# Optimization experiments

Measured on AMD Instinct MI355X. Metric: run time of the kernel, lower is better.

## Reference

```python
import jax, jax.numpy as jnp
import numpy as np

B = 16384          # batch size (positions)
NNZ_PER = 32       # active features per position (pieces on board)
F = 768            # 2 colors x 6 pieces x 64 squares
H = 512            # hidden_size


def setup_inputs() -> dict:
    key = jax.random.key(0)
    k1, k2, k3, k4, k5, k6 = jax.random.split(key, 6)
    nnz = B * NNZ_PER
    batch_row = jnp.repeat(jnp.arange(B, dtype=jnp.int64), NNZ_PER)
    stm_feat = jax.random.randint(k1, (nnz,), 0, F, dtype=jnp.int64)
    nstm_feat = jax.random.randint(k2, (nnz,), 0, F, dtype=jnp.int64)
    stm_indices = jnp.stack([batch_row, stm_feat])    # [2, nnz] COO (batch, feature)
    nstm_indices = jnp.stack([batch_row, nstm_feat])  # [2, nnz]
    stm_values = jnp.ones((nnz,), dtype=jnp.float32)   # binary features
    nstm_values = jnp.ones((nnz,), dtype=jnp.float32)
    W_ft = jax.random.normal(k3, (H, F), dtype=jnp.float32) * 0.02
    b_ft = jax.random.normal(k4, (H,), dtype=jnp.float32) * 0.02
    W_out = jax.random.normal(k5, (1, 2 * H), dtype=jnp.float32) * 0.02
    b_out = jax.random.normal(k6, (1,), dtype=jnp.float32) * 0.02
    return {
        "stm_indices": stm_indices,
        "nstm_indices": nstm_indices,
        "stm_values": stm_values,
        "nstm_values": nstm_values,
        "batch_size": B,
        "W_ft": W_ft,
        "b_ft": b_ft,
        "W_out": W_out,
        "b_out": b_out,
    }


def _to_dense(indices, values, batch_size):
    # torch.sparse_coo_tensor(...).to_dense(): duplicates are summed.
    dense = jnp.zeros((batch_size, F), dtype=jnp.float32)
    return dense.at[indices[0], indices[1]].add(values)


def reference(stm_indices, nstm_indices, stm_values, nstm_values, batch_size,
              W_ft, b_ft, W_out, b_out):
    stm_dense = _to_dense(stm_indices, stm_values, batch_size)     # [B, 768]
    nstm_dense = _to_dense(nstm_indices, nstm_values, batch_size)  # [B, 768]
    stm_hidden = stm_dense @ W_ft.T + b_ft     # [B, H]
    nstm_hidden = nstm_dense @ W_ft.T + b_ft   # [B, H]
    hidden = jnp.concatenate([stm_hidden, nstm_hidden], axis=1)  # [B, 2H]
    hidden = jnp.clip(hidden, 0.0, 1.0)
    return jax.nn.sigmoid(hidden @ W_out.T + b_out)  # [B, 1]
```

## Files before the change

kernel.cpp:

```cpp
#include <hip/hip_runtime.h>
#include <hip/hip_fp16.h>

#define B_SZ    16384
#define NNZ_PER 32
#define F_DIM   768
#define H_DIM   512
#define SLICE_H 64
#define NSLICE  8
#define CHUNK   256
#define ROWB    80

typedef unsigned int  uint32;
typedef unsigned char uchar;

#define WT8_OFF  0u
#define PK_OFF   393216u
#define PART_OFF (393216u + 4194304u)

__device__ inline uchar f32_to_e5m2(float x) {
    __half h = __float2half_rn(x);
    unsigned short hb = *(unsigned short*)&h;
    unsigned short lsb = (hb >> 8) & 1;
    hb = (unsigned short)(hb + 0x7F + lsb);
    return (uchar)(hb >> 8);
}

__global__ __launch_bounds__(256) void prep(
    const float* __restrict__ W,
    const int*   __restrict__ stm_idx,
    const int*   __restrict__ nstm_idx,
    const float* __restrict__ stm_val,
    const float* __restrict__ nstm_val,
    uchar*  __restrict__ Wt8,
    uint32* __restrict__ packed)
{
    if (blockIdx.x < 384) {
        __shared__ float tile[32][33];
        const int bx = blockIdx.x % 24;
        const int by = blockIdx.x / 24;
        const int f0 = bx * 32, h0 = by * 32;
        const int tx = threadIdx.x & 31;
        const int ty = threadIdx.x >> 5;

#pragma unroll
        for (int i = 0; i < 32; i += 8)
            tile[ty + i][tx] = W[(h0 + ty + i) * F_DIM + f0 + tx];
        __syncthreads();
        const int s = h0 >> 6;
#pragma unroll
        for (int i = 0; i < 32; i += 8) {
            const int f = f0 + ty + i;
            const int h = h0 + tx;
            Wt8[(size_t)s * (F_DIM * SLICE_H) + f * SLICE_H + (h & 63)] =
                f32_to_e5m2(tile[tx][ty + i]);
        }
    } else {
        const int e = (blockIdx.x - 384) * 256 + threadIdx.x;
        const int b = e >> 6, j = e & 63;
        const int NNZ = B_SZ * NNZ_PER;
        int f; float v;
        if (j < 32) { f = stm_idx [NNZ + b * 32 + j];        v = stm_val [b * 32 + j]; }
        else        { f = nstm_idx[NNZ + b * 32 + (j - 32)]; v = nstm_val[b * 32 + (j - 32)]; }
        __half hv = __float2half_rn(v);
        packed[e] = (uint32)(unsigned short)(f * ROWB) |
                    ((uint32)(*(unsigned short*)&hv) << 16);
    }
}

__global__ __launch_bounds__(1024, 8) void nnue_main(
    const uchar*  __restrict__ Wt8,
    const uint32* __restrict__ packed,
    const float*  __restrict__ b_ft,
    const float*  __restrict__ W_out,
    float* __restrict__ partials)
{
    __shared__ uchar Wl[F_DIM * ROWB];
    const int tid   = threadIdx.x;
    const int chunk = blockIdx.x;
    const int s     = blockIdx.y;

    {
        const uchar* src = Wt8 + (size_t)s * (F_DIM * SLICE_H);
#pragma unroll
        for (int pass = 0; pass < 3; ++pass) {
            const int o = pass * 16384 + tid * 16;
            const int f = o >> 6, col = o & 63;
            uint4 v = *(const uint4*)(src + o);
            *(uint4*)(&Wl[f * ROWB + col]) = v;
        }
    }
    __syncthreads();

    const int w    = tid >> 6;
    const int lane = tid & 63;
    const int hs   = lane & 3;
    const int pl   = lane >> 2;
    const int pos  = chunk * CHUNK + w * 16 + pl;
    const int hb   = hs * 16;

    const uint4* pk4 = (const uint4*)(packed + pos * 64);

    const uint32 selA = 0x01040004u;
    const uint32 selB = 0x03040204u;

    __half2 z = __float2half2_rn(0.f);
    __half2 sa[8] = {z,z,z,z,z,z,z,z};
    __half2 na[8] = {z,z,z,z,z,z,z,z};

#define PROC1(acc, e)                                                         \
    {                                                                         \
        const uint32 off = (e & 0xFFFFu) + (uint32)hb;                        \
        uint32 vvb = __builtin_amdgcn_perm(e, e, 0x03020302u);                \
        __half2 vv = *(__half2*)&vvb;                                         \
        uint4 wv = *(const uint4*)(&Wl[off]);                                 \
        uint32 p;                                                             \
        p = __builtin_amdgcn_perm(0u, wv.x, selA); acc[0] = __hfma2(*(__half2*)&p, vv, acc[0]); \
        p = __builtin_amdgcn_perm(0u, wv.x, selB); acc[1] = __hfma2(*(__half2*)&p, vv, acc[1]); \
        p = __builtin_amdgcn_perm(0u, wv.y, selA); acc[2] = __hfma2(*(__half2*)&p, vv, acc[2]); \
        p = __builtin_amdgcn_perm(0u, wv.y, selB); acc[3] = __hfma2(*(__half2*)&p, vv, acc[3]); \
        p = __builtin_amdgcn_perm(0u, wv.z, selA); acc[4] = __hfma2(*(__half2*)&p, vv, acc[4]); \
        p = __builtin_amdgcn_perm(0u, wv.z, selB); acc[5] = __hfma2(*(__half2*)&p, vv, acc[5]); \
        p = __builtin_amdgcn_perm(0u, wv.w, selA); acc[6] = __hfma2(*(__half2*)&p, vv, acc[6]); \
        p = __builtin_amdgcn_perm(0u, wv.w, selB); acc[7] = __hfma2(*(__half2*)&p, vv, acc[7]); \
    }

#pragma unroll
    for (int jg = 0; jg < 8; ++jg) {
        uint4 cur = pk4[jg];
        PROC1(sa, cur.x); PROC1(sa, cur.y); PROC1(sa, cur.z); PROC1(sa, cur.w);
    }
#pragma unroll
    for (int jg = 8; jg < 16; ++jg) {
        uint4 cur = pk4[jg];
        PROC1(na, cur.x); PROC1(na, cur.y); PROC1(na, cur.z); PROC1(na, cur.w);
    }
#undef PROC1

    const int h0 = s * SLICE_H + hb;
    float dot = 0.f;
#pragma unroll
    for (int i = 0; i < 8; ++i) {
        float2 bi  = *(const float2*)(b_ft  + h0 + 2 * i);
        float2 wsv = *(const float2*)(W_out + h0 + 2 * i);
        float2 wnv = *(const float2*)(W_out + H_DIM + h0 + 2 * i);
        float a0 = fminf(fmaxf(__low2float (sa[i]) + bi.x, 0.f), 1.f);
        float a1 = fminf(fmaxf(__high2float(sa[i]) + bi.y, 0.f), 1.f);
        float c0 = fminf(fmaxf(__low2float (na[i]) + bi.x, 0.f), 1.f);
        float c1 = fminf(fmaxf(__high2float(na[i]) + bi.y, 0.f), 1.f);
        dot += a0 * wsv.x + a1 * wsv.y + c0 * wnv.x + c1 * wnv.y;
    }
    dot += __shfl_xor(dot, 1, 64);
    dot += __shfl_xor(dot, 2, 64);
    if (hs == 0) partials[s * B_SZ + pos] = dot;
}

__global__ __launch_bounds__(256) void finalize(
    const float* __restrict__ partials,
    const float* __restrict__ b_out,
    float* __restrict__ out)
{
    const int b = blockIdx.x * 256 + threadIdx.x;
    float a = b_out[0];
#pragma unroll
    for (int s = 0; s < NSLICE; ++s)
        a += partials[s * B_SZ + b];
    out[b] = 1.f / (1.f + expf(-a));
}

extern "C" void kernel_launch(void* const* d_in, const int* in_sizes, int n_in,
                              void* d_out, int out_size, void* d_ws, size_t ws_size,
                              hipStream_t stream) {
    const int*   stm_idx  = (const int*)  d_in[0];
    const int*   nstm_idx = (const int*)  d_in[1];
    const float* stm_val  = (const float*)d_in[2];
    const float* nstm_val = (const float*)d_in[3];
    const float* W_ft     = (const float*)d_in[5];
    const float* b_ft     = (const float*)d_in[6];
    const float* W_out    = (const float*)d_in[7];
    const float* b_out    = (const float*)d_in[8];
    float*       out      = (float*)d_out;

    uchar*  Wt8      = (uchar*) ((char*)d_ws + WT8_OFF);
    uint32* packed   = (uint32*)((char*)d_ws + PK_OFF);
    float*  partials = (float*) ((char*)d_ws + PART_OFF);

    prep<<<384 + (B_SZ * 64) / 256, 256, 0, stream>>>(
        W_ft, stm_idx, nstm_idx, stm_val, nstm_val, Wt8, packed);

    dim3 grid(B_SZ / CHUNK, NSLICE);
    nnue_main<<<grid, 1024, 0, stream>>>(Wt8, packed, b_ft, W_out, partials);

    finalize<<<B_SZ / 256, 256, 0, stream>>>(partials, b_out, out);
}
```

Before: 105.2 us.

## Bucket features by range and process all hidden units per wave with fused finalize

The prep kernel now sorts each position's active features into six 128-feature ranges, using ballot and popcount to build per-range lists and counts. The main kernel walks the ranges, staging a 128x512 e5m2 weight tile in LDS each time. Each wave covers four positions across all 512 hidden units, broadcasting list entries with readlane and reading 8 contiguous bytes per lane from LDS. The clamp, output dot, bias and sigmoid are fused into this kernel, removing the partials buffer and the finalize launch. In exchange, each block stages the full weight matrix for only 32 positions, which raises LDS fill traffic, and any range holding more than 24 features for one side is silently truncated.

After: 125.8 us. 19.7% more time.

```diff
diff --git a/kernel.cpp b/kernel.cpp
--- a/kernel.cpp
+++ b/kernel.cpp
@@ -5,17 +5,21 @@
 #define NNZ_PER 32
 #define F_DIM   768
 #define H_DIM   512
-#define SLICE_H 64
-#define NSLICE  8
-#define CHUNK   256
-#define ROWB    80
+#define NRANGE  6
+#define RF      128
+#define CAP     24
+#define LSTRIDE 48
+#define WAVES   8
+#define PPW     4
+#define POS_PER_BLOCK (WAVES * PPW)
 
 typedef unsigned int  uint32;
+typedef unsigned long long uint64;
 typedef unsigned char uchar;
 
 #define WT8_OFF  0u
-#define PK_OFF   393216u
-#define PART_OFF (393216u + 4194304u)
+#define LIST_OFF 393216u
+#define CNT_OFF  (393216u + 18874368u)
 
 __device__ inline uchar f32_to_e5m2(float x) {
     __half h = __float2half_rn(x);
@@ -32,7 +36,8 @@
     const float* __restrict__ stm_val,
     const float* __restrict__ nstm_val,
     uchar*  __restrict__ Wt8,
-    uint32* __restrict__ packed)
+    uint32* __restrict__ lists,
+    uint32* __restrict__ counts)
 {
     if (blockIdx.x < 384) {
         __shared__ float tile[32][33];
@@ -41,130 +46,155 @@
         const int f0 = bx * 32, h0 = by * 32;
         const int tx = threadIdx.x & 31;
         const int ty = threadIdx.x >> 5;
-
 #pragma unroll
         for (int i = 0; i < 32; i += 8)
             tile[ty + i][tx] = W[(h0 + ty + i) * F_DIM + f0 + tx];
         __syncthreads();
-        const int s = h0 >> 6;
-#pragma unroll
-        for (int i = 0; i < 32; i += 8) {
-            const int f = f0 + ty + i;
-            const int h = h0 + tx;
-            Wt8[(size_t)s * (F_DIM * SLICE_H) + f * SLICE_H + (h & 63)] =
+#pragma unroll
+        for (int i = 0; i < 32; i += 8)
+            Wt8[(size_t)(f0 + ty + i) * H_DIM + (h0 + tx)] =
                 f32_to_e5m2(tile[tx][ty + i]);
-        }
     } else {
-        const int e = (blockIdx.x - 384) * 256 + threadIdx.x;
-        const int b = e >> 6, j = e & 63;
-        const int NNZ = B_SZ * NNZ_PER;
+        const int wv   = threadIdx.x >> 6;
+        const int lane = threadIdx.x & 63;
+        const int pos  = (blockIdx.x - 384) * 4 + wv;
+        const int NNZ  = B_SZ * NNZ_PER;
+
         int f; float v;
-        if (j < 32) { f = stm_idx [NNZ + b * 32 + j];        v = stm_val [b * 32 + j]; }
-        else        { f = nstm_idx[NNZ + b * 32 + (j - 32)]; v = nstm_val[b * 32 + (j - 32)]; }
+        if (lane < 32) { f = stm_idx [NNZ + pos * 32 + lane];        v = stm_val [pos * 32 + lane]; }
+        else           { f = nstm_idx[NNZ + pos * 32 + (lane - 32)]; v = nstm_val[pos * 32 + (lane - 32)]; }
+        const int range = f >> 7;
         __half hv = __float2half_rn(v);
-        packed[e] = (uint32)(unsigned short)(f * ROWB) |
-                    ((uint32)(*(unsigned short*)&hv) << 16);
-    }
-}
-
-__global__ __launch_bounds__(1024, 8) void nnue_main(
+        const uint32 packed = ((uint32)(f & 127) << 9) |
+                              ((uint32)(*(unsigned short*)&hv) << 16);
+        const uint64 below = (1ull << lane) - 1;
+
+#pragma unroll
+        for (int r = 0; r < NRANGE; ++r) {
+            const uint64 m  = __ballot(range == r);
+            const uint32 ms = (uint32)m, mn = (uint32)(m >> 32);
+            if (range == r) {
+                const uint64 lower = m & below;
+                int slot = (lane < 32) ? __popc((uint32)lower)
+                                       : (CAP + __popc((uint32)(lower >> 32)));
+                if (slot < 2 * CAP)
+                    lists[(size_t)(pos * NRANGE + r) * LSTRIDE + slot] = packed;
+            }
+            if (lane == 0) {
+                int cs = __popc(ms); if (cs > CAP) cs = CAP;
+                int cn = __popc(mn); if (cn > CAP) cn = CAP;
+                counts[pos * NRANGE + r] = (uint32)cs | ((uint32)cn << 16);
+            }
+        }
+    }
+}
+
+__global__ __launch_bounds__(512, 4) void nnue_main(
     const uchar*  __restrict__ Wt8,
-    const uint32* __restrict__ packed,
+    const uint32* __restrict__ lists,
+    const uint32* __restrict__ counts,
     const float*  __restrict__ b_ft,
     const float*  __restrict__ W_out,
-    float* __restrict__ partials)
+    const float*  __restrict__ b_out,
+    float* __restrict__ out)
 {
-    __shared__ uchar Wl[F_DIM * ROWB];
+    __shared__ uchar Wl[RF * H_DIM];
     const int tid   = threadIdx.x;
-    const int chunk = blockIdx.x;
-    const int s     = blockIdx.y;
-
-    {
-        const uchar* src = Wt8 + (size_t)s * (F_DIM * SLICE_H);
-#pragma unroll
-        for (int pass = 0; pass < 3; ++pass) {
-            const int o = pass * 16384 + tid * 16;
-            const int f = o >> 6, col = o & 63;
-            uint4 v = *(const uint4*)(src + o);
-            *(uint4*)(&Wl[f * ROWB + col]) = v;
-        }
-    }
-    __syncthreads();
-
-    const int w    = tid >> 6;
-    const int lane = tid & 63;
-    const int hs   = lane & 3;
-    const int pl   = lane >> 2;
-    const int pos  = chunk * CHUNK + w * 16 + pl;
-    const int hb   = hs * 16;
-
-    const uint4* pk4 = (const uint4*)(packed + pos * 64);
+    const int wv    = tid >> 6;
+    const int lane  = tid & 63;
+    const int pbase = blockIdx.x * POS_PER_BLOCK + wv * PPW;
+    const uint32 lane8 = (uint32)lane << 3;
 
     const uint32 selA = 0x01040004u;
     const uint32 selB = 0x03040204u;
 
     __half2 z = __float2half2_rn(0.f);
-    __half2 sa[8] = {z,z,z,z,z,z,z,z};
-    __half2 na[8] = {z,z,z,z,z,z,z,z};
-
-#define PROC1(acc, e)                                                         \
-    {                                                                         \
-        const uint32 off = (e & 0xFFFFu) + (uint32)hb;                        \
-        uint32 vvb = __builtin_amdgcn_perm(e, e, 0x03020302u);                \
-        __half2 vv = *(__half2*)&vvb;                                         \
-        uint4 wv = *(const uint4*)(&Wl[off]);                                 \
-        uint32 p;                                                             \
-        p = __builtin_amdgcn_perm(0u, wv.x, selA); acc[0] = __hfma2(*(__half2*)&p, vv, acc[0]); \
-        p = __builtin_amdgcn_perm(0u, wv.x, selB); acc[1] = __hfma2(*(__half2*)&p, vv, acc[1]); \
-        p = __builtin_amdgcn_perm(0u, wv.y, selA); acc[2] = __hfma2(*(__half2*)&p, vv, acc[2]); \
-        p = __builtin_amdgcn_perm(0u, wv.y, selB); acc[3] = __hfma2(*(__half2*)&p, vv, acc[3]); \
-        p = __builtin_amdgcn_perm(0u, wv.z, selA); acc[4] = __hfma2(*(__half2*)&p, vv, acc[4]); \
-        p = __builtin_amdgcn_perm(0u, wv.z, selB); acc[5] = __hfma2(*(__half2*)&p, vv, acc[5]); \
-        p = __builtin_amdgcn_perm(0u, wv.w, selA); acc[6] = __hfma2(*(__half2*)&p, vv, acc[6]); \
-        p = __builtin_amdgcn_perm(0u, wv.w, selB); acc[7] = __hfma2(*(__half2*)&p, vv, acc[7]); \
-    }
-
-#pragma unroll
-    for (int jg = 0; jg < 8; ++jg) {
-        uint4 cur = pk4[jg];
-        PROC1(sa, cur.x); PROC1(sa, cur.y); PROC1(sa, cur.z); PROC1(sa, cur.w);
-    }
-#pragma unroll
-    for (int jg = 8; jg < 16; ++jg) {
-        uint4 cur = pk4[jg];
-        PROC1(na, cur.x); PROC1(na, cur.y); PROC1(na, cur.z); PROC1(na, cur.w);
-    }
-#undef PROC1
-
-    const int h0 = s * SLICE_H + hb;
-    float dot = 0.f;
-#pragma unroll
-    for (int i = 0; i < 8; ++i) {
-        float2 bi  = *(const float2*)(b_ft  + h0 + 2 * i);
-        float2 wsv = *(const float2*)(W_out + h0 + 2 * i);
-        float2 wnv = *(const float2*)(W_out + H_DIM + h0 + 2 * i);
-        float a0 = fminf(fmaxf(__low2float (sa[i]) + bi.x, 0.f), 1.f);
-        float a1 = fminf(fmaxf(__high2float(sa[i]) + bi.y, 0.f), 1.f);
-        float c0 = fminf(fmaxf(__low2float (na[i]) + bi.x, 0.f), 1.f);
-        float c1 = fminf(fmaxf(__high2float(na[i]) + bi.y, 0.f), 1.f);
-        dot += a0 * wsv.x + a1 * wsv.y + c0 * wnv.x + c1 * wnv.y;
-    }
-    dot += __shfl_xor(dot, 1, 64);
-    dot += __shfl_xor(dot, 2, 64);
-    if (hs == 0) partials[s * B_SZ + pos] = dot;
-}
-
-__global__ __launch_bounds__(256) void finalize(
-    const float* __restrict__ partials,
-    const float* __restrict__ b_out,
-    float* __restrict__ out)
-{
-    const int b = blockIdx.x * 256 + threadIdx.x;
-    float a = b_out[0];
-#pragma unroll
-    for (int s = 0; s < NSLICE; ++s)
-        a += partials[s * B_SZ + b];
-    out[b] = 1.f / (1.f + expf(-a));
+    __half2 sa[PPW][4], na[PPW][4];
+#pragma unroll
+    for (int p = 0; p < PPW; ++p)
+#pragma unroll
+        for (int k = 0; k < 4; ++k) { sa[p][k] = z; na[p][k] = z; }
+
+    for (int r = 0; r < NRANGE; ++r) {
+        __syncthreads();
+        {
+            const uchar* src = Wt8 + (size_t)r * (RF * H_DIM);
+#pragma unroll
+            for (int i = 0; i < 8; ++i) {
+                const int o = i * 8192 + tid * 16;
+                *(uint4*)(Wl + o) = *(const uint4*)(src + o);
+            }
+        }
+        __syncthreads();
+
+        uint32 cw[PPW], el[PPW];
+#pragma unroll
+        for (int p = 0; p < PPW; ++p) {
+            const int pr = (pbase + p) * NRANGE + r;
+            cw[p] = counts[pr];
+            el[p] = 0;
+            if (lane < 2 * CAP) el[p] = lists[(size_t)pr * LSTRIDE + lane];
+        }
+
+#pragma unroll
+        for (int p = 0; p < PPW; ++p) {
+            int cs = (int)(cw[p] & 0xFFFFu);  if (cs > CAP) cs = CAP;
+            int cn = (int)(cw[p] >> 16);      if (cn > CAP) cn = CAP;
+
+            for (int j = 0; j < cs; ++j) {
+                const uint32 e   = __builtin_amdgcn_readlane(el[p], j);
+                const uint32 off = e & 0xFFFFu;
+                uint32 vvb = (e & 0xFFFF0000u) | (e >> 16);
+                __half2 vv = *(__half2*)&vvb;
+                uint2 w2 = *(const uint2*)(Wl + off + lane8);
+                uint32 q;
+                q = __builtin_amdgcn_perm(0u, w2.x, selA); sa[p][0] = __hfma2(*(__half2*)&q, vv, sa[p][0]);
+                q = __builtin_amdgcn_perm(0u, w2.x, selB); sa[p][1] = __hfma2(*(__half2*)&q, vv, sa[p][1]);
+                q = __builtin_amdgcn_perm(0u, w2.y, selA); sa[p][2] = __hfma2(*(__half2*)&q, vv, sa[p][2]);
+                q = __builtin_amdgcn_perm(0u, w2.y, selB); sa[p][3] = __hfma2(*(__half2*)&q, vv, sa[p][3]);
+            }
+            for (int j = 0; j < cn; ++j) {
+                const uint32 e   = __builtin_amdgcn_readlane(el[p], CAP + j);
+                const uint32 off = e & 0xFFFFu;
+                uint32 vvb = (e & 0xFFFF0000u) | (e >> 16);
+                __half2 vv = *(__half2*)&vvb;
+                uint2 w2 = *(const uint2*)(Wl + off + lane8);
+                uint32 q;
+                q = __builtin_amdgcn_perm(0u, w2.x, selA); na[p][0] = __hfma2(*(__half2*)&q, vv, na[p][0]);
+                q = __builtin_amdgcn_perm(0u, w2.x, selB); na[p][1] = __hfma2(*(__half2*)&q, vv, na[p][1]);
+                q = __builtin_amdgcn_perm(0u, w2.y, selA); na[p][2] = __hfma2(*(__half2*)&q, vv, na[p][2]);
+                q = __builtin_amdgcn_perm(0u, w2.y, selB); na[p][3] = __hfma2(*(__half2*)&q, vv, na[p][3]);
+            }
+        }
+    }
+
+    const int h0 = lane * 8;
+    float2 bi[4], wsv[4], wnv[4];
+#pragma unroll
+    for (int k = 0; k < 4; ++k) {
+        bi[k]  = *(const float2*)(b_ft  + h0 + 2 * k);
+        wsv[k] = *(const float2*)(W_out + h0 + 2 * k);
+        wnv[k] = *(const float2*)(W_out + H_DIM + h0 + 2 * k);
+    }
+    const float bo = b_out[0];
+
+#pragma unroll
+    for (int p = 0; p < PPW; ++p) {
+        float dot = 0.f;
+#pragma unroll
+        for (int k = 0; k < 4; ++k) {
+            float a0 = fminf(fmaxf(__low2float (sa[p][k]) + bi[k].x, 0.f), 1.f);
+            float a1 = fminf(fmaxf(__high2float(sa[p][k]) + bi[k].y, 0.f), 1.f);
+            float c0 = fminf(fmaxf(__low2float (na[p][k]) + bi[k].x, 0.f), 1.f);
+            float c1 = fminf(fmaxf(__high2float(na[p][k]) + bi[k].y, 0.f), 1.f);
+            dot += a0 * wsv[k].x + a1 * wsv[k].y + c0 * wnv[k].x + c1 * wnv[k].y;
+        }
+#pragma unroll
+        for (int off = 32; off > 0; off >>= 1)
+            dot += __shfl_xor(dot, off, 64);
+        if (lane == 0)
+            out[pbase + p] = 1.f / (1.f + expf(-(dot + bo)));
+    }
 }
 
 extern "C" void kernel_launch(void* const* d_in, const int* in_sizes, int n_in,
@@ -180,15 +210,13 @@
     const float* b_out    = (const float*)d_in[8];
     float*       out      = (float*)d_out;
 
-    uchar*  Wt8      = (uchar*) ((char*)d_ws + WT8_OFF);
-    uint32* packed   = (uint32*)((char*)d_ws + PK_OFF);
-    float*  partials = (float*) ((char*)d_ws + PART_OFF);
-
-    prep<<<384 + (B_SZ * 64) / 256, 256, 0, stream>>>(
-        W_ft, stm_idx, nstm_idx, stm_val, nstm_val, Wt8, packed);
-
-    dim3 grid(B_SZ / CHUNK, NSLICE);
-    nnue_main<<<grid, 1024, 0, stream>>>(Wt8, packed, b_ft, W_out, partials);
-
-    finalize<<<B_SZ / 256, 256, 0, stream>>>(partials, b_out, out);
-}
+    uchar*  Wt8    = (uchar*) ((char*)d_ws + WT8_OFF);
+    uint32* lists  = (uint32*)((char*)d_ws + LIST_OFF);
+    uint32* counts = (uint32*)((char*)d_ws + CNT_OFF);
+
+    prep<<<384 + B_SZ / 4, 256, 0, stream>>>(
+        W_ft, stm_idx, nstm_idx, stm_val, nstm_val, Wt8, lists, counts);
+
+    nnue_main<<<B_SZ / POS_PER_BLOCK, 512, 0, stream>>>(
+        Wt8, lists, counts, b_ft, W_out, b_out, out);
+}
```
